# Optimization experiments

Measured on AMD Instinct MI355X. Metric: run time of the kernel, lower is better.

The kernel has to match this reference:

```python
import jax, jax.numpy as jnp
import numpy as np

N_ATOMS = 200000   # total atoms across batch of molecules
N_BONDS = 400000   # total directed bonds
HSIZE   = 256      # mpn_size
MLP     = 512      # mlp_size
BS_OUT  = 5        # bond edit classes (bs_outdim)
N_MOLS  = 1000     # batch of molecules (len(atom_scope))


def _p(k, shape, scale):
    return jax.random.normal(k, shape, jnp.float32) * scale


def setup_inputs() -> dict:
    key = jax.random.key(0)
    ks = jax.random.split(key, 12)
    s_h = 1.0 / np.sqrt(HSIZE).astype(np.float32)
    s_2h = 1.0 / np.sqrt(2 * HSIZE).astype(np.float32)
    s_m = 1.0 / np.sqrt(MLP).astype(np.float32)
    return {
        'c_atom':  jax.random.normal(ks[0], (N_ATOMS, HSIZE), jnp.float32),
        'ha_prev': jax.random.normal(ks[1], (N_ATOMS, HSIZE), jnp.float32),
        'W_vv':    jnp.eye(HSIZE, dtype=jnp.float32),  # nn.init.eye_ in original
        'W_vc':    _p(ks[2], (HSIZE, HSIZE), s_h),
        'bond_W1': _p(ks[3], (2 * HSIZE, MLP), s_2h),
        'bond_b1': jnp.zeros((MLP,), jnp.float32),
        'bond_W2': _p(ks[4], (MLP, BS_OUT), s_m),
        'bond_b2': jnp.zeros((BS_OUT,), jnp.float32),
        'uni_W1':  _p(ks[5], (HSIZE, MLP), s_h),
        'uni_b1':  jnp.zeros((MLP,), jnp.float32),
        'uni_W2':  _p(ks[6], (MLP, 1), s_m),
        'uni_b2':  jnp.zeros((1,), jnp.float32),
        'done_W1': _p(ks[7], (HSIZE, MLP), s_h),
        'done_b1': jnp.zeros((MLP,), jnp.float32),
        'done_W2': _p(ks[8], (MLP, 1), s_m),
        'done_b2': jnp.zeros((1,), jnp.float32),
        'mol_id':     jax.random.randint(ks[9], (N_ATOMS,), 0, N_MOLS, jnp.int32),
        'bond_index': jax.random.randint(ks[10], (N_BONDS, 2), 0, N_ATOMS, jnp.int32),
    }


def _mlp(x, W1, b1, W2, b2):
    # build_mlp: Linear -> ReLU -> (dropout, off at eval) -> Linear
    return jax.nn.relu(x @ W1 + b1) @ W2 + b2


def reference(c_atom, ha_prev, W_vv, W_vc,
              bond_W1, bond_b1, bond_W2, bond_b2,
              uni_W1, uni_b1, uni_W2, uni_b2,
              done_W1, done_b1, done_W2, done_b2,
              mol_id, bond_index):
    # ha = relu(W_vv @ ha_prev + W_vc @ c_atom); ha[0] = 0 (padding atom)
    ha = jax.nn.relu(ha_prev @ W_vv + c_atom @ W_vc)
    ha = ha.at[0].set(0.0)
    # per-molecule pooling (replaces python loop over atom_scope)
    hm = jax.ops.segment_sum(ha, mol_id, num_segments=N_MOLS)  # [N_MOLS, H]
    # gather bond endpoint embeddings (index_select_ND)
    bond_in = jnp.concatenate([ha[bond_index[:, 0]], ha[bond_index[:, 1]]], axis=-1)  # [E, 2H]
    bond_logits = _mlp(bond_in, bond_W1, bond_b1, bond_W2, bond_b2)  # [E, BS_OUT]
    uni_logits = _mlp(ha, uni_W1, uni_b1, uni_W2, uni_b2)            # [N, 1]
    done_logits = _mlp(hm, done_W1, done_b1, done_W2, done_b2)       # [M, 1]
    # edit_logits in original is a ragged per-mol concat of these three;
    # return the dense flat concatenation (same values, fixed shape)
    return jnp.concatenate([bond_logits.ravel(), uni_logits.ravel(), done_logits.ravel()])
```

## Files before the change

kernel.cpp:

```cpp
#include <hip/hip_runtime.h>
#include <hip/hip_bf16.h>
#include <math.h>

typedef __attribute__((ext_vector_type(8))) short bf16x8;
typedef __attribute__((ext_vector_type(4))) float f32x4;

static __device__ __forceinline__ unsigned short f2bf(float f) {
    union { float f; unsigned u; } v; v.f = f;
    unsigned r = v.u + 0x7fffu + ((v.u >> 16) & 1u);
    return (unsigned short)(r >> 16);
}
static __device__ __forceinline__ float bf2f(unsigned short b) {
    union { unsigned u; float f; } v; v.u = ((unsigned)b) << 16;
    return v.f;
}

#define GLOAD16(g, l) __builtin_amdgcn_global_load_lds( \
    (const __attribute__((address_space(1))) void*)(g), \
    (__attribute__((address_space(3))) void*)(l), 16, 0, 0)

#if defined(__has_builtin)
#  if __has_builtin(__builtin_amdgcn_cvt_pk_fp8_f32) && __has_builtin(__builtin_amdgcn_cvt_pk_f32_fp8)
#    define HAVE_FP8_CVT 1
#  endif
#endif
#ifndef HAVE_FP8_CVT
#  define HAVE_FP8_CVT 0
#endif

static __device__ __forceinline__ float f8dec_sw(unsigned b) {
    unsigned s = b >> 7, e = (b >> 3) & 15, m = b & 7;
    float v = e ? ldexpf((float)(8 + m), (int)e - 10) : ldexpf((float)m, -9);
    return s ? -v : v;
}
static __device__ __forceinline__ unsigned char f8enc_sw(float x) {
    union { float f; unsigned u; } v; v.f = x;
    unsigned s = (v.u >> 31) << 7;
    float ax = fabsf(x);
    if (ax >= 448.f) return (unsigned char)(s | 0x7E);
    if (ax < 0.015625f) { int m = (int)(ax * 512.f + 0.5f); return (unsigned char)(s | m); }
    int e; float fr = frexpf(ax, &e);
    int q = (int)(fr * 16.f + 0.5f);
    if (q == 16) { q = 8; e += 1; }
    if (e - 1 > 8) return (unsigned char)(s | 0x7E);
    return (unsigned char)(s | ((e - 1 + 7) << 3) | (q - 8));
}
static __device__ __forceinline__ unsigned char f8e(float v) {
#if HAVE_FP8_CVT
    return (unsigned char)(__builtin_amdgcn_cvt_pk_fp8_f32(v, v, 0, false) & 0xFF);
#else
    return f8enc_sw(v);
#endif
}
static __device__ __forceinline__ void f8d2_lo(unsigned w, float& x, float& y) {
#if HAVE_FP8_CVT
    auto r = __builtin_amdgcn_cvt_pk_f32_fp8((int)w, false);
    x = r[0]; y = r[1];
#else
    x = f8dec_sw(w & 0xFF); y = f8dec_sw((w >> 8) & 0xFF);
#endif
}
static __device__ __forceinline__ void f8d2_hi(unsigned w, float& x, float& y) {
#if HAVE_FP8_CVT
    auto r = __builtin_amdgcn_cvt_pk_f32_fp8((int)w, true);
    x = r[0]; y = r[1];
#else
    x = f8dec_sw((w >> 16) & 0xFF); y = f8dec_sw((w >> 24) & 0xFF);
#endif
}

__global__ __launch_bounds__(256) void conv_weights(
    const float* __restrict__ Wvv, const float* __restrict__ Wvc,
    const float* __restrict__ bW1, const float* __restrict__ uW1,
    unsigned short* __restrict__ WcT, unsigned short* __restrict__ WgT)
{
    int idx = blockIdx.x * 256 + threadIdx.x;
    if (idx < 131072) {
        int n = idx & 255, k = idx >> 8;
        float s = (k < 256) ? Wvv[k * 256 + n] : Wvc[(k - 256) * 256 + n];
        WcT[((k >> 3) * 256 + n) * 8 + (k & 7)] = f2bf(s);
    } else {
        int t = idx - 131072;
        int k = t / 1536, n2 = t - k * 1536;
        float s;
        if (n2 < 512)       s = bW1[k * 512 + n2];
        else if (n2 < 1024) s = bW1[(256 + k) * 512 + (n2 - 512)];
        else                s = uW1[k * 512 + (n2 - 1024)];
        WgT[((k >> 3) * 1536 + n2) * 8 + (k & 7)] = f2bf(s);
    }
}

__global__ __launch_bounds__(512, 4) void ha_kernel(
    const float* __restrict__ ha_prev, const float* __restrict__ c_atom,
    const unsigned short* __restrict__ WcT,
    unsigned short* __restrict__ haB, int NA)
{
    __shared__ __align__(16) unsigned short As[2][128 * 64];

    const int tid = threadIdx.x;
    const int wv = tid >> 6, lane = tid & 63;
    const int wr = wv >> 2, wc = wv & 3;
    const int c15 = lane & 15, kq = lane >> 4;
    const int xm3 = (c15 & 7) << 3;
    const int m0 = blockIdx.x * 128;

    const int cr0 = tid >> 3, chc = tid & 7;
    const int cr1 = (512 + tid) >> 3;
    int row0 = m0 + cr0; if (row0 >= NA) row0 = NA - 1;
    int row1 = m0 + cr1; if (row1 >= NA) row1 = NA - 1;

    f32x4 v00, v01, v10, v11;
    #define HA_LOAD(ks) { \
        const float* src = ((ks) < 4) ? ha_prev : c_atom; \
        const int kb = ((ks) & 3) * 64 + chc * 8; \
        const float* s0 = src + (size_t)row0 * 256 + kb; \
        const float* s1 = src + (size_t)row1 * 256 + kb; \
        v00 = *(const f32x4*)s0; v01 = *(const f32x4*)(s0 + 4); \
        v10 = *(const f32x4*)s1; v11 = *(const f32x4*)(s1 + 4); }
    #define HA_WRITE(buf) { \
        bf16x8 p0, p1; \
        p0[0]=(short)f2bf(v00[0]); p0[1]=(short)f2bf(v00[1]); p0[2]=(short)f2bf(v00[2]); p0[3]=(short)f2bf(v00[3]); \
        p0[4]=(short)f2bf(v01[0]); p0[5]=(short)f2bf(v01[1]); p0[6]=(short)f2bf(v01[2]); p0[7]=(short)f2bf(v01[3]); \
        p1[0]=(short)f2bf(v10[0]); p1[1]=(short)f2bf(v10[1]); p1[2]=(short)f2bf(v10[2]); p1[3]=(short)f2bf(v10[3]); \
        p1[4]=(short)f2bf(v11[0]); p1[5]=(short)f2bf(v11[1]); p1[6]=(short)f2bf(v11[2]); p1[7]=(short)f2bf(v11[3]); \
        *(bf16x8*)&As[buf][cr0 * 64 + ((chc * 8) ^ ((cr0 & 7) << 3))] = p0; \
        *(bf16x8*)&As[buf][cr1 * 64 + ((chc * 8) ^ ((cr1 & 7) << 3))] = p1; }

    f32x4 acc[4][4];
#pragma unroll
    for (int m = 0; m < 4; ++m)
#pragma unroll
        for (int n = 0; n < 4; ++n) acc[m][n] = (f32x4){0.f, 0.f, 0.f, 0.f};

    HA_LOAD(0); HA_WRITE(0);
    __syncthreads();

    for (int ks = 0; ks < 8; ++ks) {
        if (ks < 7) HA_LOAD(ks + 1);
        const int buf = ks & 1;
#pragma unroll
        for (int kk = 0; kk < 2; ++kk) {
            bf16x8 aF[4], bF[4];
            const int plane = ks * 8 + kk * 4 + kq;
#pragma unroll
            for (int n = 0; n < 4; ++n)
                bF[n] = *(const bf16x8*)(WcT + ((size_t)plane * 256 + wc * 64 + n * 16 + c15) * 8);
#pragma unroll
            for (int m = 0; m < 4; ++m)
                aF[m] = *(const bf16x8*)&As[buf][(wr * 64 + m * 16 + c15) * 64 + ((kk * 32 + kq * 8) ^ xm3)];
#pragma unroll
            for (int m = 0; m < 4; ++m)
#pragma unroll
                for (int n = 0; n < 4; ++n)
                    acc[m][n] = __builtin_amdgcn_mfma_f32_16x16x32_bf16(aF[m], bF[n], acc[m][n], 0, 0, 0);
        }
        if (ks < 7) HA_WRITE((ks + 1) & 1);
        __syncthreads();
    }

#pragma unroll
    for (int m = 0; m < 4; ++m) {
#pragma unroll
        for (int reg = 0; reg < 4; ++reg) {
            int row = m0 + wr * 64 + m * 16 + kq * 4 + reg;
            if (row >= NA) continue;
            bool z = (row == 0);
#pragma unroll
            for (int n = 0; n < 4; ++n) {
                int col = wc * 64 + n * 16 + c15;
                float v = fmaxf(acc[m][n][reg], 0.f);
                if (z) v = 0.f;
                haB[(size_t)row * 256 + col] = f2bf(v);
            }
        }
    }
}

__global__ __launch_bounds__(1024, 4) void g_kernel(
    const unsigned short* __restrict__ haB, const unsigned short* __restrict__ WgT,
    const int* __restrict__ mol_id, float* __restrict__ hm,
    unsigned char* __restrict__ G, float* __restrict__ outU,
    const float* __restrict__ ub1, const float* __restrict__ uW2,
    const float* __restrict__ ub2, int NA)
{
    __shared__ __align__(16) unsigned short As[4][128][64];
    __shared__ float obuf[128];
    __shared__ int molS[128];

    const int tid = threadIdx.x;
    const int wv = tid >> 6, lane = tid & 63;
    const int wr = wv >> 3, wc = wv & 7;
    const int c15 = lane & 15, kq = lane >> 4;
    const int a0 = blockIdx.x * 128;
    const int nb = blockIdx.y;

    if (tid < 128) {
        obuf[tid] = 0.f;
        molS[tid] = (a0 + tid < NA) ? mol_id[a0 + tid] : 0;
    }
    {
        const int kt = wv >> 2;
        const int rsub = lane >> 3, csub = lane & 7;
#pragma unroll
        for (int j = 0; j < 4; ++j) {
            int rg = (wv & 3) * 4 + j;
            int r = rg * 8 + rsub;
            int ga = a0 + r; if (ga >= NA) ga = NA - 1;
            GLOAD16(haB + (size_t)ga * 256 + kt * 64 + (size_t)((csub ^ (r & 7)) * 8),
                    &As[kt][rg * 8][0]);
        }
    }
    __syncthreads();

    f32x4 acc[4][4];
#pragma unroll
    for (int m = 0; m < 4; ++m)
#pragma unroll
        for (int n = 0; n < 4; ++n) acc[m][n] = (f32x4){0.f, 0.f, 0.f, 0.f};

    bf16x8 breg[2][4];
#pragma unroll
    for (int n = 0; n < 4; ++n)
        breg[0][n] = *(const bf16x8*)(WgT + ((size_t)kq * 1536 + nb * 512 + wc * 64 + n * 16 + c15) * 8);

#pragma unroll
    for (int s = 0; s < 8; ++s) {
        if (s < 7) {
            const int pl = (s + 1) * 4 + kq;
#pragma unroll
            for (int n = 0; n < 4; ++n)
                breg[(s + 1) & 1][n] = *(const bf16x8*)(WgT + ((size_t)pl * 1536 + nb * 512 + wc * 64 + n * 16 + c15) * 8);
        }
        const int ks = s >> 1, kk = s & 1;
        bf16x8 aF[4];
#pragma unroll
        for (int m = 0; m < 4; ++m) {
            int r = wr * 64 + m * 16 + c15;
            aF[m] = *(const bf16x8*)&As[ks][r][((kk * 4 + kq) ^ (r & 7)) * 8];
        }
#pragma unroll
        for (int m = 0; m < 4; ++m)
#pragma unroll
            for (int n = 0; n < 4; ++n)
                acc[m][n] = __builtin_amdgcn_mfma_f32_16x16x32_bf16(aF[m], breg[s & 1][n], acc[m][n], 0, 0, 0);
    }

    if (nb < 2) {
#pragma unroll
        for (int m = 0; m < 4; ++m) {
#pragma unroll
            for (int reg = 0; reg < 4; ++reg) {
                int row = a0 + wr * 64 + m * 16 + kq * 4 + reg;
                if (row >= NA) continue;
#pragma unroll
                for (int n = 0; n < 4; ++n) {
                    int col = wc * 64 + n * 16 + c15;
                    G[(size_t)row * 1024 + nb * 512 + col] = f8e(acc[m][n][reg]);
                }
            }
        }
    } else {
        float b1c[4], w2c[4];
#pragma unroll
        for (int n = 0; n < 4; ++n) {
            int col = wc * 64 + n * 16 + c15;
            b1c[n] = ub1[col];
            w2c[n] = uW2[col];
        }
#pragma unroll
        for (int m = 0; m < 4; ++m) {
#pragma unroll
            for (int reg = 0; reg < 4; ++reg) {
                float s0 = 0.f;
#pragma unroll
                for (int n = 0; n < 4; ++n)
                    s0 += fmaxf(acc[m][n][reg] + b1c[n], 0.f) * w2c[n];
#pragma unroll
                for (int off = 1; off < 16; off <<= 1) s0 += __shfl_xor(s0, off);
                if (c15 == 0)
                    atomicAdd(&obuf[wr * 64 + m * 16 + kq * 4 + reg], s0);
            }
        }
        __syncthreads();
        if (tid < 128) {
            int row = a0 + tid;
            if (row < NA) outU[row] = obuf[tid] + ub2[0];
        }
    }

    {
        const int c0 = nb * 86;
        const int c1 = (c0 + 86 < 256) ? c0 + 86 : 256;
        const int rgp = tid >> 7, tc = tid & 127;
        const int c = c0 + tc;
        if (c < c1) {
            const int kt2 = c >> 6, q = (c & 63) >> 3, jj = c & 7;
#pragma unroll 4
            for (int rr = rgp; rr < 128; rr += 8) {
                int row = a0 + rr;
                if (row > 0 && row < NA) {
                    float v = bf2f(As[kt2][rr][((q ^ (rr & 7)) << 3) + jj]);
                    if (v != 0.f) atomicAdd(&hm[molS[rr] * 256 + c], v);
                }
            }
        }
    }
}

__global__ __launch_bounds__(256) void bond_stream(
    const unsigned char* __restrict__ G, const int* __restrict__ bidx,
    const float* __restrict__ b1, const float* __restrict__ W2,
    const float* __restrict__ b2, float* __restrict__ outB, int NB, int nwaves)
{
    const int lane = threadIdx.x & 63;
    const int wid = (blockIdx.x * blockDim.x + threadIdx.x) >> 6;

    float b1c[8], w2c[8][5];
#pragma unroll
    for (int i = 0; i < 8; ++i) {
        int h = lane * 8 + i;
        b1c[i] = b1[h];
#pragma unroll
        for (int j = 0; j < 5; ++j) w2c[i][j] = W2[h * 5 + j];
    }
    float bb[5];
#pragma unroll
    for (int j = 0; j < 5; ++j) bb[j] = b2[j];

    int e = wid;
    if (e >= NB) return;
    int2 ep = ((const int2*)bidx)[e];
    int2 epN = (e + nwaves < NB) ? ((const int2*)bidx)[e + nwaves] : ep;
    uint2 ga = *(const uint2*)(G + (size_t)ep.x * 1024 + lane * 8);
    uint2 gb = *(const uint2*)(G + (size_t)ep.y * 1024 + 512 + lane * 8);

    while (e < NB) {
        int en = e + nwaves;
        uint2 gaN, gbN; int2 epN2 = epN;
        if (en < NB) {
            gaN = *(const uint2*)(G + (size_t)epN.x * 1024 + lane * 8);
            gbN = *(const uint2*)(G + (size_t)epN.y * 1024 + 512 + lane * 8);
            int e2 = en + nwaves;
            if (e2 < NB) epN2 = ((const int2*)bidx)[e2];
        }
        float s[5] = {0.f, 0.f, 0.f, 0.f, 0.f};
#pragma unroll
        for (int half = 0; half < 2; ++half) {
            unsigned wa = half ? ga.y : ga.x;
            unsigned wb = half ? gb.y : gb.x;
            float a0v, a1v, a2v, a3v, b0v, b1v, b2v, b3v;
            f8d2_lo(wa, a0v, a1v); f8d2_hi(wa, a2v, a3v);
            f8d2_lo(wb, b0v, b1v); f8d2_hi(wb, b2v, b3v);
            float hv[4] = { a0v + b0v, a1v + b1v, a2v + b2v, a3v + b3v };
#pragma unroll
            for (int t = 0; t < 4; ++t) {
                int i = half * 4 + t;
                float p = fmaxf(hv[t] + b1c[i], 0.f);
#pragma unroll
                for (int j = 0; j < 5; ++j) s[j] += p * w2c[i][j];
            }
        }
#pragma unroll
        for (int off = 1; off < 64; off <<= 1)
#pragma unroll
            for (int j = 0; j < 5; ++j) s[j] += __shfl_xor(s[j], off);
        if (lane == 0) {
#pragma unroll
            for (int j = 0; j < 5; ++j) outB[(size_t)e * 5 + j] = s[j] + bb[j];
        }
        e = en; ga = gaN; gb = gbN; epN = epN2;
    }
}

__global__ __launch_bounds__(256) void hm_fallback(
    const unsigned short* __restrict__ haB, const int* __restrict__ mol_id,
    float* __restrict__ hm, int NA)
{
    int idx = blockIdx.x * 256 + threadIdx.x;
    int row = idx >> 6, c4 = (idx & 63) * 4;
    if (row == 0 || row >= NA) return;
    int mol = mol_id[row];
    const unsigned short* p = haB + (size_t)row * 256 + c4;
#pragma unroll
    for (int j = 0; j < 4; ++j) {
        float v = bf2f(p[j]);
        if (v != 0.f) atomicAdd(&hm[mol * 256 + c4 + j], v);
    }
}

__global__ __launch_bounds__(512, 4) void bond_gemm(
    const unsigned short* __restrict__ haB, const int* __restrict__ bidx,
    const unsigned short* __restrict__ WgT, const float* __restrict__ b1,
    const float* __restrict__ W2, const float* __restrict__ b2,
    float* __restrict__ outB, int NB)
{
    __shared__ __align__(16) unsigned short As[8 * 64 * 64];
    __shared__ float obuf[64][5];

    const int tid = threadIdx.x;
    const int wv = tid >> 6, lane = tid & 63;
    const int c15 = lane & 15, kq = lane >> 4;
    const int b0 = blockIdx.x * 64;

    if (tid < 320) ((float*)obuf)[tid] = 0.f;

    {
        const int ep = wv >> 2, koff = (wv & 3) * 64;
        const int rsub = lane >> 3, csub = lane & 7;
        int eidxs[8];
#pragma unroll
        for (int j = 0; j < 8; ++j) {
            int gbd = b0 + j * 8 + rsub; if (gbd >= NB) gbd = 0;
            eidxs[j] = bidx[gbd * 2 + ep];
        }
#pragma unroll
        for (int j = 0; j < 8; ++j) {
            int r = j * 8 + rsub;
            GLOAD16(haB + (size_t)eidxs[j] * 256 + koff + (size_t)((csub ^ (r & 7)) * 8),
                    As + wv * 4096 + j * 512);
        }
    }
    __syncthreads();

    f32x4 acc[4][4];
#pragma unroll
    for (int m = 0; m < 4; ++m)
#pragma unroll
        for (int n = 0; n < 4; ++n) acc[m][n] = (f32x4){0.f, 0.f, 0.f, 0.f};

#pragma unroll 1
    for (int s = 0; s < 16; ++s) {
        const int pl = s * 4 + kq;
        bf16x8 br[4], aF[4];
#pragma unroll
        for (int n = 0; n < 4; ++n)
            br[n] = *(const bf16x8*)(WgT + ((size_t)(pl & 31) * 1536 + (pl >> 5) * 512 + wv * 64 + n * 16 + c15) * 8);
        const int ks = s >> 1, kk = s & 1;
#pragma unroll
        for (int m = 0; m < 4; ++m) {
            int r = m * 16 + c15;
            aF[m] = *(const bf16x8*)&As[ks * 4096 + r * 64 + (((kk * 4 + kq) ^ (r & 7)) * 8)];
        }
#pragma unroll
        for (int m = 0; m < 4; ++m)
#pragma unroll
            for (int n = 0; n < 4; ++n)
                acc[m][n] = __builtin_amdgcn_mfma_f32_16x16x32_bf16(aF[m], br[n], acc[m][n], 0, 0, 0);
    }

    float b1c[4], w2c[4][5];
#pragma unroll
    for (int n = 0; n < 4; ++n) {
        int col = wv * 64 + n * 16 + c15;
        b1c[n] = b1[col];
#pragma unroll
        for (int j = 0; j < 5; ++j) w2c[n][j] = W2[col * 5 + j];
    }
#pragma unroll
    for (int m = 0; m < 4; ++m) {
#pragma unroll
        for (int reg = 0; reg < 4; ++reg) {
            float s[5] = {0.f, 0.f, 0.f, 0.f, 0.f};
#pragma unroll
            for (int n = 0; n < 4; ++n) {
                float p = fmaxf(acc[m][n][reg] + b1c[n], 0.f);
#pragma unroll
                for (int j = 0; j < 5; ++j) s[j] += p * w2c[n][j];
            }
#pragma unroll
            for (int off = 1; off < 16; off <<= 1)
#pragma unroll
                for (int j = 0; j < 5; ++j) s[j] += __shfl_xor(s[j], off);
            if (c15 == 0) {
                int rl = m * 16 + kq * 4 + reg;
#pragma unroll
                for (int j = 0; j < 5; ++j) atomicAdd(&obuf[rl][j], s[j]);
            }
        }
    }
    __syncthreads();
    {
        int r = tid >> 3, j = tid & 7;
        if (j < 5) {
            int row = b0 + r;
            if (row < NB) outB[(size_t)row * 5 + j] = obuf[r][j] + b2[j];
        }
    }
}

__global__ __launch_bounds__(512, 4) void uni_kernel(
    const unsigned short* __restrict__ haB, const unsigned short* __restrict__ WgT,
    const float* __restrict__ b1, const float* __restrict__ W2,
    const float* __restrict__ b2, float* __restrict__ outU, int NA)
{
    __shared__ __align__(16) unsigned short As[4 * 64 * 64];
    __shared__ float obuf[64];

    const int tid = threadIdx.x;
    const int wv = tid >> 6, lane = tid & 63;
    const int c15 = lane & 15, kq = lane >> 4;
    const int a0 = blockIdx.x * 64;

    if (tid < 64) obuf[tid] = 0.f;

    {
        const int kt = wv >> 1, koff = kt * 64;
        const int rsub = lane >> 3, csub = lane & 7;
#pragma unroll
        for (int jj = 0; jj < 4; ++jj) {
            int j = (wv & 1) * 4 + jj;
            int r = j * 8 + rsub;
            int ga = a0 + r; if (ga >= NA) ga = NA - 1;
            GLOAD16(haB + (size_t)ga * 256 + koff + (size_t)((csub ^ (r & 7)) * 8),
                    As + kt * 4096 + j * 512);
        }
    }
    __syncthreads();

    f32x4 acc[4][4];
#pragma unroll
    for (int m = 0; m < 4; ++m)
#pragma unroll
        for (int n = 0; n < 4; ++n) acc[m][n] = (f32x4){0.f, 0.f, 0.f, 0.f};

#pragma unroll 1
    for (int s = 0; s < 8; ++s) {
        const int pl = s * 4 + kq;
        bf16x8 br[4], aF[4];
#pragma unroll
        for (int n = 0; n < 4; ++n)
            br[n] = *(const bf16x8*)(WgT + ((size_t)pl * 1536 + 1024 + wv * 64 + n * 16 + c15) * 8);
        const int ks = s >> 1, kk = s & 1;
#pragma unroll
        for (int m = 0; m < 4; ++m) {
            int r = m * 16 + c15;
            aF[m] = *(const bf16x8*)&As[ks * 4096 + r * 64 + (((kk * 4 + kq) ^ (r & 7)) * 8)];
        }
#pragma unroll
        for (int m = 0; m < 4; ++m)
#pragma unroll
            for (int n = 0; n < 4; ++n)
                acc[m][n] = __builtin_amdgcn_mfma_f32_16x16x32_bf16(aF[m], br[n], acc[m][n], 0, 0, 0);
    }

    float b1c[4], w2c[4];
#pragma unroll
    for (int n = 0; n < 4; ++n) {
        int col = wv * 64 + n * 16 + c15;
        b1c[n] = b1[col];
        w2c[n] = W2[col];
    }
#pragma unroll
    for (int m = 0; m < 4; ++m) {
#pragma unroll
        for (int reg = 0; reg < 4; ++reg) {
            float s = 0.f;
#pragma unroll
            for (int n = 0; n < 4; ++n)
                s += fmaxf(acc[m][n][reg] + b1c[n], 0.f) * w2c[n];
#pragma unroll
            for (int off = 1; off < 16; off <<= 1) s += __shfl_xor(s, off);
            if (c15 == 0) atomicAdd(&obuf[m * 16 + kq * 4 + reg], s);
        }
    }
    __syncthreads();
    if (tid < 64) {
        int row = a0 + tid;
        if (row < NA) outU[row] = obuf[tid] + b2[0];
    }
}

__global__ __launch_bounds__(256) void done_kernel(
    const float* __restrict__ hm, const float* __restrict__ W1,
    const float* __restrict__ b1, const float* __restrict__ W2,
    const float* __restrict__ b2, float* __restrict__ outD, int NM)
{
    __shared__ float rsh[4][256];
    __shared__ float red[4][4];
    const int tid = threadIdx.x;
    const int wv = tid >> 6, lane = tid & 63;
    const int mol0 = blockIdx.x * 4;
#pragma unroll
    for (int q = 0; q < 4; ++q)
        rsh[q][tid] = (mol0 + q < NM) ? hm[(size_t)(mol0 + q) * 256 + tid] : 0.f;
    __syncthreads();
    float h[4][2];
#pragma unroll
    for (int q = 0; q < 4; ++q) { h[q][0] = 0.f; h[q][1] = 0.f; }
    for (int k = 0; k < 256; ++k) {
        float w0 = W1[k * 512 + tid];
        float w1 = W1[k * 512 + tid + 256];
#pragma unroll
        for (int q = 0; q < 4; ++q) {
            h[q][0] += rsh[q][k] * w0;
            h[q][1] += rsh[q][k] * w1;
        }
    }
    float bb0 = b1[tid], bb1v = b1[tid + 256];
    float ww0 = W2[tid], ww1 = W2[tid + 256];
#pragma unroll
    for (int q = 0; q < 4; ++q) {
        float p = fmaxf(h[q][0] + bb0, 0.f) * ww0 + fmaxf(h[q][1] + bb1v, 0.f) * ww1;
#pragma unroll
        for (int off = 1; off < 64; off <<= 1) p += __shfl_xor(p, off);
        if (lane == 0) red[q][wv] = p;
    }
    __syncthreads();
    if (tid < 4 && mol0 + tid < NM)
        outD[mol0 + tid] = red[tid][0] + red[tid][1] + red[tid][2] + red[tid][3] + b2[0];
}

extern "C" void kernel_launch(void* const* d_in, const int* in_sizes, int n_in,
                              void* d_out, int out_size, void* d_ws, size_t ws_size,
                              hipStream_t stream)
{
    const float* c_atom  = (const float*)d_in[0];
    const float* ha_prev = (const float*)d_in[1];
    const float* W_vv    = (const float*)d_in[2];
    const float* W_vc    = (const float*)d_in[3];
    const float* bW1     = (const float*)d_in[4];
    const float* bb1     = (const float*)d_in[5];
    const float* bW2     = (const float*)d_in[6];
    const float* bb2     = (const float*)d_in[7];
    const float* uW1     = (const float*)d_in[8];
    const float* ub1     = (const float*)d_in[9];
    const float* uW2     = (const float*)d_in[10];
    const float* ub2     = (const float*)d_in[11];
    const float* dW1     = (const float*)d_in[12];
    const float* db1     = (const float*)d_in[13];
    const float* dW2     = (const float*)d_in[14];
    const float* db2     = (const float*)d_in[15];
    const int* mol_id    = (const int*)d_in[16];
    const int* bidx      = (const int*)d_in[17];

    const int H = 256, BS = 5;
    const int NA = in_sizes[0] / H;
    const int NB = in_sizes[17] / 2;
    const int NM = out_size - NB * BS - NA;

    float* out  = (float*)d_out;
    float* outB = out;
    float* outU = out + (size_t)NB * BS;
    float* outD = outU + NA;

    char* ws = (char*)d_ws;
    size_t off = 0;
    unsigned short* haB = (unsigned short*)(ws + off);
    off += (size_t)NA * H * 2;            off = (off + 255) & ~(size_t)255;
    float* hm = (float*)(ws + off);
    off += (size_t)NM * H * 4;            off = (off + 255) & ~(size_t)255;
    unsigned short* WcT = (unsigned short*)(ws + off);
    off += (size_t)131072 * 2;            off = (off + 255) & ~(size_t)255;
    unsigned short* WgT = (unsigned short*)(ws + off);
    off += (size_t)393216 * 2;            off = (off + 255) & ~(size_t)255;
    unsigned char* G = (unsigned char*)(ws + off);
    size_t need_G = off + (size_t)NA * 1024;

    const bool hasG = ws_size >= need_G;

    hipMemsetAsync(hm, 0, (size_t)NM * H * 4, stream);
    conv_weights<<<2048, 256, 0, stream>>>(W_vv, W_vc, bW1, uW1, WcT, WgT);
    ha_kernel<<<(NA + 127) / 128, 512, 0, stream>>>(ha_prev, c_atom, WcT, haB, NA);

    if (hasG) {
        g_kernel<<<dim3((NA + 127) / 128, 3), 1024, 0, stream>>>(
            haB, WgT, mol_id, hm, G, outU, ub1, uW2, ub2, NA);
        bond_stream<<<2048, 256, 0, stream>>>(G, bidx, bb1, bW2, bb2, outB, NB, 2048 * 4);
    } else {
        hm_fallback<<<(NA * 64 + 255) / 256, 256, 0, stream>>>(haB, mol_id, hm, NA);
        bond_gemm<<<(NB + 63) / 64, 512, 0, stream>>>(haB, bidx, WgT, bb1, bW2, bb2, outB, NB);
        uni_kernel<<<(NA + 63) / 64, 512, 0, stream>>>(haB, WgT, ub1, uW2, ub2, outU, NA);
    }
    done_kernel<<<(NM + 3) / 4, 256, 0, stream>>>(hm, dW1, db1, dW2, db2, outD, NM);
}
```

Before: 651.2 us.

## Replace atomic hm pooling with sort-by-molecule segmented reduction; deepen bond prefetch

The per-atom float atomicAdd pooling into hm inside g_kernel is replaced by a counting sort of atoms by molecule (histogram, single-block scan, scatter) and a per-molecule hm_kernel that sums bf16 rows without atomics. The bond_stream loop is also restructured to prefetch two edges ahead instead of one, with clamped indices in place of branches. This removes roughly 50M global atomics but adds four small kernels, including a serial single-block scan, plus a gather pass over haB. hm_kernel does not skip atom 0, but ha row 0 is already zeroed in ha_kernel, so results should match.

```diff
diff --git a/kernel.cpp b/kernel.cpp
--- a/kernel.cpp
+++ b/kernel.cpp
@@ -87,6 +87,83 @@
         else if (n2 < 1024) s = bW1[(256 + k) * 512 + (n2 - 512)];
         else                s = uW1[k * 512 + (n2 - 1024)];
         WgT[((k >> 3) * 1536 + n2) * 8 + (k & 7)] = f2bf(s);
+    }
+}
+
+__global__ __launch_bounds__(256) void hist_kernel(
+    const int* __restrict__ mol_id, int* __restrict__ bins, int NA)
+{
+    int i = blockIdx.x * 256 + threadIdx.x;
+    if (i < NA) atomicAdd(&bins[mol_id[i]], 1);
+}
+
+__global__ __launch_bounds__(1024) void scan_kernel(
+    const int* __restrict__ bins, int* __restrict__ offs,
+    int* __restrict__ cursor, int NM)
+{
+    __shared__ int buf[1024];
+    const int t = threadIdx.x;
+    int base = 0;
+    for (int c0 = 0; c0 < NM; c0 += 1024) {
+        int v = (c0 + t < NM) ? bins[c0 + t] : 0;
+        buf[t] = v;
+        __syncthreads();
+        for (int d = 1; d < 1024; d <<= 1) {
+            int x = (t >= d) ? buf[t - d] : 0;
+            __syncthreads();
+            buf[t] += x;
+            __syncthreads();
+        }
+        int incl = buf[t];
+        if (c0 + t < NM) {
+            int ex = base + incl - v;
+            offs[c0 + t] = ex;
+            cursor[c0 + t] = ex;
+        }
+        int tot = buf[1023];
+        __syncthreads();
+        base += tot;
+    }
+    if (t == 0) offs[NM] = base;
+}
+
+__global__ __launch_bounds__(256) void scatter_kernel(
+    const int* __restrict__ mol_id, int* __restrict__ cursor,
+    int* __restrict__ sorted, int NA)
+{
+    int i = blockIdx.x * 256 + threadIdx.x;
+    if (i < NA) {
+        int p = atomicAdd(&cursor[mol_id[i]], 1);
+        sorted[p] = i;
+    }
+}
+
+__global__ __launch_bounds__(256) void hm_kernel(
+    const unsigned short* __restrict__ haB, const int* __restrict__ sorted,
+    const int* __restrict__ offs, float* __restrict__ hm, int NM)
+{
+    __shared__ float red[256][2];
+    const int mol = blockIdx.x;
+    const int t = threadIdx.x;
+    const int sub = t >> 7, cp = t & 127;
+    const int s0 = offs[mol], s1 = offs[mol + 1];
+    float a0 = 0.f, a1 = 0.f;
+    for (int i = s0 + sub; i < s1; i += 2) {
+        int a = sorted[i];
+        unsigned w = *(const unsigned*)(haB + (size_t)a * 256 + cp * 2);
+        union { unsigned u; float f; } lo, hi;
+        lo.u = w << 16;
+        hi.u = w & 0xFFFF0000u;
+        a0 += lo.f;
+        a1 += hi.f;
+    }
+    red[t][0] = a0; red[t][1] = a1;
+    __syncthreads();
+    if (t < 128) {
+        float r0 = red[t][0] + red[t + 128][0];
+        float r1 = red[t][1] + red[t + 128][1];
+        float2* dst = (float2*)&hm[(size_t)mol * 256 + cp * 2];
+        *dst = make_float2(r0, r1);
     }
 }
 
@@ -178,14 +255,12 @@
 
 __global__ __launch_bounds__(1024, 4) void g_kernel(
     const unsigned short* __restrict__ haB, const unsigned short* __restrict__ WgT,
-    const int* __restrict__ mol_id, float* __restrict__ hm,
     unsigned char* __restrict__ G, float* __restrict__ outU,
     const float* __restrict__ ub1, const float* __restrict__ uW2,
     const float* __restrict__ ub2, int NA)
 {
     __shared__ __align__(16) unsigned short As[4][128][64];
     __shared__ float obuf[128];
-    __shared__ int molS[128];
 
     const int tid = threadIdx.x;
     const int wv = tid >> 6, lane = tid & 63;
@@ -194,10 +269,7 @@
     const int a0 = blockIdx.x * 128;
     const int nb = blockIdx.y;
 
-    if (tid < 128) {
-        obuf[tid] = 0.f;
-        molS[tid] = (a0 + tid < NA) ? mol_id[a0 + tid] : 0;
-    }
+    if (tid < 128) obuf[tid] = 0.f;
     {
         const int kt = wv >> 2;
         const int rsub = lane >> 3, csub = lane & 7;
@@ -287,24 +359,6 @@
             if (row < NA) outU[row] = obuf[tid] + ub2[0];
         }
     }
-
-    {
-        const int c0 = nb * 86;
-        const int c1 = (c0 + 86 < 256) ? c0 + 86 : 256;
-        const int rgp = tid >> 7, tc = tid & 127;
-        const int c = c0 + tc;
-        if (c < c1) {
-            const int kt2 = c >> 6, q = (c & 63) >> 3, jj = c & 7;
-#pragma unroll 4
-            for (int rr = rgp; rr < 128; rr += 8) {
-                int row = a0 + rr;
-                if (row > 0 && row < NA) {
-                    float v = bf2f(As[kt2][rr][((q ^ (rr & 7)) << 3) + jj]);
-                    if (v != 0.f) atomicAdd(&hm[molS[rr] * 256 + c], v);
-                }
-            }
-        }
-    }
 }
 
 __global__ __launch_bounds__(256) void bond_stream(
@@ -327,27 +381,32 @@
 #pragma unroll
     for (int j = 0; j < 5; ++j) bb[j] = b2[j];
 
+    if (wid >= NB) return;
+    const int last = NB - 1;
+    const int goff = lane * 8;
+
     int e = wid;
-    if (e >= NB) return;
-    int2 ep = ((const int2*)bidx)[e];
-    int2 epN = (e + nwaves < NB) ? ((const int2*)bidx)[e + nwaves] : ep;
-    uint2 ga = *(const uint2*)(G + (size_t)ep.x * 1024 + lane * 8);
-    uint2 gb = *(const uint2*)(G + (size_t)ep.y * 1024 + 512 + lane * 8);
-
-    while (e < NB) {
-        int en = e + nwaves;
-        uint2 gaN, gbN; int2 epN2 = epN;
-        if (en < NB) {
-            gaN = *(const uint2*)(G + (size_t)epN.x * 1024 + lane * 8);
-            gbN = *(const uint2*)(G + (size_t)epN.y * 1024 + 512 + lane * 8);
-            int e2 = en + nwaves;
-            if (e2 < NB) epN2 = ((const int2*)bidx)[e2];
-        }
+    int e1 = e + nwaves;  if (e1 > last) e1 = last;
+    int e2 = e1 + nwaves; if (e2 > last) e2 = last;
+    int2 p0 = ((const int2*)bidx)[e];
+    int2 p1 = ((const int2*)bidx)[e1];
+    int2 p2 = ((const int2*)bidx)[e2];
+    uint2 ga0 = *(const uint2*)(G + (size_t)p0.x * 1024 + goff);
+    uint2 gb0 = *(const uint2*)(G + (size_t)p0.y * 1024 + 512 + goff);
+    uint2 ga1 = *(const uint2*)(G + (size_t)p1.x * 1024 + goff);
+    uint2 gb1 = *(const uint2*)(G + (size_t)p1.y * 1024 + 512 + goff);
+
+    while (true) {
+        uint2 ga2 = *(const uint2*)(G + (size_t)p2.x * 1024 + goff);
+        uint2 gb2 = *(const uint2*)(G + (size_t)p2.y * 1024 + 512 + goff);
+        int e3 = e2 + nwaves; if (e3 > last) e3 = last;
+        int2 p3 = ((const int2*)bidx)[e3];
+
         float s[5] = {0.f, 0.f, 0.f, 0.f, 0.f};
 #pragma unroll
         for (int half = 0; half < 2; ++half) {
-            unsigned wa = half ? ga.y : ga.x;
-            unsigned wb = half ? gb.y : gb.x;
+            unsigned wa = half ? ga0.y : ga0.x;
+            unsigned wb = half ? gb0.y : gb0.x;
             float a0v, a1v, a2v, a3v, b0v, b1v, b2v, b3v;
             f8d2_lo(wa, a0v, a1v); f8d2_hi(wa, a2v, a3v);
             f8d2_lo(wb, b0v, b1v); f8d2_hi(wb, b2v, b3v);
@@ -368,7 +427,11 @@
 #pragma unroll
             for (int j = 0; j < 5; ++j) outB[(size_t)e * 5 + j] = s[j] + bb[j];
         }
-        e = en; ga = gaN; gb = gbN; epN = epN2;
+        e += nwaves;
+        if (e > last) break;
+        ga0 = ga1; gb0 = gb1;
+        ga1 = ga2; gb1 = gb2;
+        p2 = p3; e2 = e3;
     }
 }
 
@@ -653,20 +716,34 @@
     off += (size_t)131072 * 2;            off = (off + 255) & ~(size_t)255;
     unsigned short* WgT = (unsigned short*)(ws + off);
     off += (size_t)393216 * 2;            off = (off + 255) & ~(size_t)255;
+    int* bins = (int*)(ws + off);
+    off += (size_t)NM * 4;                off = (off + 255) & ~(size_t)255;
+    int* cursor = (int*)(ws + off);
+    off += (size_t)NM * 4;                off = (off + 255) & ~(size_t)255;
+    int* offs = (int*)(ws + off);
+    off += (size_t)(NM + 1) * 4;          off = (off + 255) & ~(size_t)255;
+    int* sorted = (int*)(ws + off);
+    off += (size_t)NA * 4;                off = (off + 255) & ~(size_t)255;
     unsigned char* G = (unsigned char*)(ws + off);
     size_t need_G = off + (size_t)NA * 1024;
 
     const bool hasG = ws_size >= need_G;
 
-    hipMemsetAsync(hm, 0, (size_t)NM * H * 4, stream);
     conv_weights<<<2048, 256, 0, stream>>>(W_vv, W_vc, bW1, uW1, WcT, WgT);
-    ha_kernel<<<(NA + 127) / 128, 512, 0, stream>>>(ha_prev, c_atom, WcT, haB, NA);
 
     if (hasG) {
+        hipMemsetAsync(bins, 0, (size_t)NM * 4, stream);
+        hist_kernel<<<(NA + 255) / 256, 256, 0, stream>>>(mol_id, bins, NA);
+        scan_kernel<<<1, 1024, 0, stream>>>(bins, offs, cursor, NM);
+        scatter_kernel<<<(NA + 255) / 256, 256, 0, stream>>>(mol_id, cursor, sorted, NA);
+        ha_kernel<<<(NA + 127) / 128, 512, 0, stream>>>(ha_prev, c_atom, WcT, haB, NA);
+        hm_kernel<<<NM, 256, 0, stream>>>(haB, sorted, offs, hm, NM);
         g_kernel<<<dim3((NA + 127) / 128, 3), 1024, 0, stream>>>(
-            haB, WgT, mol_id, hm, G, outU, ub1, uW2, ub2, NA);
+            haB, WgT, G, outU, ub1, uW2, ub2, NA);
         bond_stream<<<2048, 256, 0, stream>>>(G, bidx, bb1, bW2, bb2, outB, NB, 2048 * 4);
     } else {
+        hipMemsetAsync(hm, 0, (size_t)NM * H * 4, stream);
+        ha_kernel<<<(NA + 127) / 128, 512, 0, stream>>>(ha_prev, c_atom, WcT, haB, NA);
         hm_fallback<<<(NA * 64 + 255) / 256, 256, 0, stream>>>(haB, mol_id, hm, NA);
         bond_gemm<<<(NB + 63) / 64, 512, 0, stream>>>(haB, bidx, WgT, bb1, bW2, bb2, outB, NB);
         uni_kernel<<<(NA + 63) / 64, 512, 0, stream>>>(haB, WgT, ub1, uW2, ub2, outU, NA);
```

New measurement: 680.2 us. 1.04x slower.
